# Kernel optimization log

Measured on AMD Instinct MI355X. Metric: run time of the kernel, lower is better.

## Reference

```python
import jax, jax.numpy as jnp
import numpy as np

N = 16384   # nodes at current level
M = 8192    # nodes at next (coarser) level
E = 524288  # edges (avg degree 32)
D = 128     # in_feats == out_feats
LN_EPS = 1e-5


def setup_inputs() -> dict:
    key = jax.random.key(0)
    ks = jax.random.split(key, 10)
    curr_h = jax.random.normal(ks[0], (N, D), jnp.float32)
    next_h = jax.random.normal(ks[1], (M, D), jnp.float32)
    curr_inc = jax.random.uniform(ks[2], (N, M), jnp.float32)
    edge_src = jax.random.randint(ks[3], (E,), 0, N, jnp.int32)
    edge_dst = jax.random.randint(ks[4], (E,), 0, N, jnp.int32)
    Wc = jax.random.normal(ks[5], (D, D), jnp.float32) / np.float32(np.sqrt(D))
    Wf = jax.random.normal(ks[6], (D, D), jnp.float32) / np.float32(np.sqrt(D))
    bc = jnp.zeros((D,), jnp.float32)
    bf = jnp.zeros((D,), jnp.float32)
    conv_w = jax.random.uniform(ks[7], (D,), jnp.float32)
    topDown_w = jax.random.uniform(ks[8], (D,), jnp.float32)
    gamma = jnp.ones((D,), jnp.float32)
    beta = jnp.zeros((D,), jnp.float32)
    return dict(curr_h=curr_h, next_h=next_h, curr_inc=curr_inc,
                Wc=Wc, bc=bc, Wf=Wf, bf=bf, conv_w=conv_w,
                topDown_w=topDown_w, gamma=gamma, beta=beta,
                edge_src=edge_src, edge_dst=edge_dst)


def _graph_conv(x, W, b, src, dst, n):
    # DGL GraphConv, norm='both', on graph with self-loops added.
    ones = jnp.ones(src.shape[0], x.dtype)
    out_deg = jax.ops.segment_sum(ones, src, num_segments=n) + 1.0  # +1 self-loop
    in_deg = jax.ops.segment_sum(ones, dst, num_segments=n) + 1.0
    xn = x * jax.lax.rsqrt(out_deg)[:, None]
    # neighbor SpMM + self-loop contribution
    agg = jax.ops.segment_sum(xn[src], dst, num_segments=n) + xn
    agg = agg * jax.lax.rsqrt(in_deg)[:, None]
    return agg @ W + b


def reference(curr_h, next_h, curr_inc, Wc, bc, Wf, bf, conv_w,
              topDown_w, gamma, beta, edge_src, edge_dst):
    n = curr_h.shape[0]
    conv_layer = _graph_conv(curr_h, Wc, bc, edge_src, edge_dst, n) * conv_w[None, :]
    fused_in = curr_inc @ next_h  # dense incidence matmul [N, D]
    top_down = _graph_conv(fused_in, Wf, bf, edge_src, edge_dst, n) * topDown_w[None, :]
    res = (conv_layer + top_down) * 0.5  # update == 'MEAN' over stack of 2
    # LayerNorm over feature dim
    mu = jnp.mean(res, axis=-1, keepdims=True)
    var = jnp.mean(jnp.square(res - mu), axis=-1, keepdims=True)
    res = (res - mu) * jax.lax.rsqrt(var + LN_EPS) * gamma + beta
    res = jax.nn.relu(res)  # activation == 'RELU'
    # dropout: eval mode -> identity
    return res
```

## Files before the change

kernel.cpp:

```cpp
#include <hip/hip_runtime.h>

constexpr int Nn = 16384;
constexpr int Mm = 8192;
constexpr int Ee = 524288;
constexpr int Dd = 128;

typedef __attribute__((ext_vector_type(8))) short short8v;
typedef __attribute__((ext_vector_type(4))) short short4v;
typedef __attribute__((ext_vector_type(4))) float float4v;

static __device__ __forceinline__ short f2bf(float f) {
    unsigned u = __builtin_bit_cast(unsigned, f);
    u += 0x7fffu + ((u >> 16) & 1u);
    return (short)(u >> 16);
}

__global__ void k_zero_i(int* __restrict__ p, int n) {
    int i = blockIdx.x * 256 + threadIdx.x;
    if (i < n) p[i] = 0;
}

__global__ void k_deg_count(const int* __restrict__ src, const int* __restrict__ dst,
                            int* __restrict__ cnt_out, int* __restrict__ cnt_in) {
    int e = blockIdx.x * 256 + threadIdx.x;
    if (e < Ee) {
        atomicAdd(&cnt_out[src[e]], 1);
        atomicAdd(&cnt_in[dst[e]], 1);
    }
}

__global__ void k_deg_fin(const int* __restrict__ cnt_out, const int* __restrict__ cnt_in,
                          float* __restrict__ rs_out, float* __restrict__ rs_in) {
    int i = blockIdx.x * 256 + threadIdx.x;
    if (i < Nn) {
        rs_out[i] = rsqrtf((float)(cnt_out[i] + 1));
        rs_in[i]  = rsqrtf((float)(cnt_in[i] + 1));
    }
}

__global__ void k_scan(const int* __restrict__ cnt, int* __restrict__ row_start) {
    __shared__ int s[1024];
    int t = threadIdx.x;
    int base = t * 16;
    int local[16];
    int sum = 0;
#pragma unroll
    for (int i = 0; i < 16; i++) { local[i] = cnt[base + i]; sum += local[i]; }
    s[t] = sum;
    __syncthreads();
    for (int off = 1; off < 1024; off <<= 1) {
        int v = (t >= off) ? s[t - off] : 0;
        __syncthreads();
        s[t] += v;
        __syncthreads();
    }
    int run = s[t] - sum;
#pragma unroll
    for (int i = 0; i < 16; i++) { row_start[base + i] = run; run += local[i]; }
    if (t == 1023) row_start[16384] = s[1023];
}

__global__ void k_fill(const int* __restrict__ src, const int* __restrict__ dst,
                       const int* __restrict__ row_start, int* __restrict__ cursor,
                       int* __restrict__ ebuf) {
    int e = blockIdx.x * 256 + threadIdx.x;
    if (e < Ee) {
        int d = dst[e];
        int pos = atomicAdd(&cursor[d], 1);
        ebuf[row_start[d] + pos] = src[e];
    }
}

__global__ void k_agg(const float* __restrict__ x, const float* __restrict__ rs_o,
                      const float* __restrict__ rs_i, const int* __restrict__ row_start,
                      const int* __restrict__ ebuf, float* __restrict__ agg) {
    int d = blockIdx.x * 4 + (threadIdx.x >> 6);
    int lane = threadIdx.x & 63;
    int c = lane * 2;
    int beg = row_start[d], end = row_start[d + 1];
    float ax = 0.f, ay = 0.f;
    int i = beg;
    for (; i + 1 < end; i += 2) {
        int s0 = ebuf[i], s1 = ebuf[i + 1];
        float r0 = rs_o[s0], r1 = rs_o[s1];
        float2 v0 = *(const float2*)(x + (size_t)s0 * 128 + c);
        float2 v1 = *(const float2*)(x + (size_t)s1 * 128 + c);
        ax += v0.x * r0 + v1.x * r1;
        ay += v0.y * r0 + v1.y * r1;
    }
    if (i < end) {
        int s0 = ebuf[i];
        float r0 = rs_o[s0];
        float2 v0 = *(const float2*)(x + (size_t)s0 * 128 + c);
        ax += v0.x * r0;
        ay += v0.y * r0;
    }
    float2 vs = *(const float2*)(x + (size_t)d * 128 + c);
    float ro = rs_o[d], ri = rs_i[d];
    float2 o;
    o.x = (ax + vs.x * ro) * ri;
    o.y = (ay + vs.y * ro) * ri;
    *(float2*)(agg + (size_t)d * 128 + c) = o;
}

__global__ void k_bt(const float* __restrict__ B, short* __restrict__ Bt) {
    __shared__ short T[32][40];
    int kt = blockIdx.x & 255;
    int nt = blockIdx.x >> 8;
    int t = threadIdx.x;
    int r = t >> 3;
    int c4 = (t & 7) * 4;
    float4 v = *(const float4*)(B + (size_t)(kt * 32 + r) * 128 + nt * 32 + c4);
    T[c4 + 0][r] = f2bf(v.x);
    T[c4 + 1][r] = f2bf(v.y);
    T[c4 + 2][r] = f2bf(v.z);
    T[c4 + 3][r] = f2bf(v.w);
    __syncthreads();
    int nl = t >> 3, ks = (t & 7) * 4;
    *(short4v*)(Bt + (size_t)(nt * 32 + nl) * 8192 + kt * 32 + ks) =
        *(const short4v*)(&T[nl][ks]);
}

__launch_bounds__(256, 2)
__global__ void k_mfma_gemm(const float* __restrict__ A, const short* __restrict__ Bt,
                            float* __restrict__ C) {
    __shared__ short As[32 * 72];
    __shared__ short Bs[128 * 72];

    const int tid = threadIdx.x;
    const int lane = tid & 63;
    const int wv = tid >> 6;
    const int row0 = blockIdx.x * 32;

    const int ar = tid >> 3;
    const int ak = (tid & 7) * 8;
    const float* Ap = A + (size_t)(row0 + ar) * Mm + ak;

    const int bn = tid >> 1;
    const int bk = (tid & 1) * 32;
    const short* Bp = Bt + (size_t)bn * Mm + bk;

    const int fm = lane & 15;
    const int fk = (lane >> 4) * 8;

    float4v acc[2][2] = {};

    for (int k0 = 0; k0 < Mm; k0 += 64) {
        float4 a0 = *(const float4*)(Ap + k0);
        float4 a1 = *(const float4*)(Ap + k0 + 4);
        short8v b0 = *(const short8v*)(Bp + k0);
        short8v b1 = *(const short8v*)(Bp + k0 + 8);
        short8v b2 = *(const short8v*)(Bp + k0 + 16);
        short8v b3 = *(const short8v*)(Bp + k0 + 24);
        __syncthreads();
        short8v ap;
        ap[0] = f2bf(a0.x); ap[1] = f2bf(a0.y); ap[2] = f2bf(a0.z); ap[3] = f2bf(a0.w);
        ap[4] = f2bf(a1.x); ap[5] = f2bf(a1.y); ap[6] = f2bf(a1.z); ap[7] = f2bf(a1.w);
        *(short8v*)(&As[ar * 72 + ak]) = ap;
        *(short8v*)(&Bs[bn * 72 + bk +  0]) = b0;
        *(short8v*)(&Bs[bn * 72 + bk +  8]) = b1;
        *(short8v*)(&Bs[bn * 72 + bk + 16]) = b2;
        *(short8v*)(&Bs[bn * 72 + bk + 24]) = b3;
        __syncthreads();
#pragma unroll
        for (int ks = 0; ks < 2; ks++) {
            const int kk = ks * 32 + fk;
            short8v a0f = *(const short8v*)(&As[fm * 72 + kk]);
            short8v a1f = *(const short8v*)(&As[(16 + fm) * 72 + kk]);
            short8v b0f = *(const short8v*)(&Bs[(wv * 32 + fm) * 72 + kk]);
            short8v b1f = *(const short8v*)(&Bs[(wv * 32 + 16 + fm) * 72 + kk]);
            acc[0][0] = __builtin_amdgcn_mfma_f32_16x16x32_bf16(a0f, b0f, acc[0][0], 0, 0, 0);
            acc[0][1] = __builtin_amdgcn_mfma_f32_16x16x32_bf16(a0f, b1f, acc[0][1], 0, 0, 0);
            acc[1][0] = __builtin_amdgcn_mfma_f32_16x16x32_bf16(a1f, b0f, acc[1][0], 0, 0, 0);
            acc[1][1] = __builtin_amdgcn_mfma_f32_16x16x32_bf16(a1f, b1f, acc[1][1], 0, 0, 0);
        }
    }

    const int crow = (lane >> 4) * 4;
#pragma unroll
    for (int mt = 0; mt < 2; mt++)
#pragma unroll
        for (int nt = 0; nt < 2; nt++)
#pragma unroll
            for (int r = 0; r < 4; r++)
                C[(size_t)(row0 + mt * 16 + crow + r) * 128 + wv * 32 + nt * 16 + fm] =
                    acc[mt][nt][r];
}

__launch_bounds__(256, 2)
__global__ void k_gemm(const float* __restrict__ A, const float* __restrict__ B,
                       float* __restrict__ C, int K,
                       const float* __restrict__ bias, const float* __restrict__ scale,
                       const float* __restrict__ prev, int mode) {
    __shared__ float As[32 * 36];
    __shared__ float Bs[32 * 128];

    const int tid = threadIdx.x;
    const int tx = tid & 31;
    const int ty = tid >> 5;
    const int c4 = tx * 4;
    const int r0 = ty * 4;
    const int row0 = blockIdx.x * 32;

    const int ar = tid >> 3;
    const int ak = (tid & 7) * 4;
    const float* Arow = A + (size_t)(row0 + ar) * K + ak;

    float acc[4][4] = {};

    for (int k0 = 0; k0 < K; k0 += 32) {
        float4 av = *(const float4*)(Arow + k0);
        float4 bv[4];
#pragma unroll
        for (int t = 0; t < 4; t++) {
            int idx = tid + t * 256;
            int br = idx >> 5, bc = (idx & 31) * 4;
            bv[t] = *(const float4*)(B + (size_t)(k0 + br) * 128 + bc);
        }
        __syncthreads();
        As[(ak + 0) * 36 + ar] = av.x;
        As[(ak + 1) * 36 + ar] = av.y;
        As[(ak + 2) * 36 + ar] = av.z;
        As[(ak + 3) * 36 + ar] = av.w;
#pragma unroll
        for (int t = 0; t < 4; t++) {
            int idx = tid + t * 256;
            int br = idx >> 5, bc = (idx & 31) * 4;
            *(float4*)(Bs + br * 128 + bc) = bv[t];
        }
        __syncthreads();
#pragma unroll
        for (int kk = 0; kk < 32; kk++) {
            float4 a4 = *(const float4*)(As + kk * 36 + r0);
            float4 b4 = *(const float4*)(Bs + kk * 128 + c4);
            float a[4] = {a4.x, a4.y, a4.z, a4.w};
            float b[4] = {b4.x, b4.y, b4.z, b4.w};
#pragma unroll
            for (int i = 0; i < 4; i++)
#pragma unroll
                for (int j = 0; j < 4; j++)
                    acc[i][j] = fmaf(a[i], b[j], acc[i][j]);
        }
    }

    float4 bi = *(const float4*)(bias + c4);
    float4 sc = *(const float4*)(scale + c4);
#pragma unroll
    for (int i = 0; i < 4; i++) {
        size_t o = (size_t)(row0 + r0 + i) * 128 + c4;
        float4 v = {acc[i][0], acc[i][1], acc[i][2], acc[i][3]};
        v.x = (v.x + bi.x) * sc.x;
        v.y = (v.y + bi.y) * sc.y;
        v.z = (v.z + bi.z) * sc.z;
        v.w = (v.w + bi.w) * sc.w;
        if (mode == 2) {
            float4 p = *(const float4*)(prev + o);
            v.x = (v.x + p.x) * 0.5f;
            v.y = (v.y + p.y) * 0.5f;
            v.z = (v.z + p.z) * 0.5f;
            v.w = (v.w + p.w) * 0.5f;
        }
        *(float4*)(C + o) = v;
    }
}

__global__ void k_ln_relu(const float* __restrict__ x, const float* __restrict__ gamma,
                          const float* __restrict__ beta, float* __restrict__ out) {
    int wave = threadIdx.x >> 6;
    int lane = threadIdx.x & 63;
    int row = blockIdx.x * 4 + wave;
    const float* xr = x + (size_t)row * 128;
    float2 v = *(const float2*)(xr + lane * 2);
    float s1 = v.x + v.y;
    float s2 = v.x * v.x + v.y * v.y;
#pragma unroll
    for (int m = 32; m >= 1; m >>= 1) {
        s1 += __shfl_xor(s1, m);
        s2 += __shfl_xor(s2, m);
    }
    float mu = s1 * (1.0f / 128.0f);
    float var = s2 * (1.0f / 128.0f) - mu * mu;
    float inv = rsqrtf(var + 1e-5f);
    float2 g = *(const float2*)(gamma + lane * 2);
    float2 b = *(const float2*)(beta + lane * 2);
    float2 o;
    o.x = fmaxf((v.x - mu) * inv * g.x + b.x, 0.0f);
    o.y = fmaxf((v.y - mu) * inv * g.y + b.y, 0.0f);
    *(float2*)(out + (size_t)row * 128 + lane * 2) = o;
}

extern "C" void kernel_launch(void* const* d_in, const int* in_sizes, int n_in,
                              void* d_out, int out_size, void* d_ws, size_t ws_size,
                              hipStream_t stream) {
    const float* curr_h    = (const float*)d_in[0];
    const float* next_h    = (const float*)d_in[1];
    const float* curr_inc  = (const float*)d_in[2];
    const float* Wc        = (const float*)d_in[3];
    const float* bc        = (const float*)d_in[4];
    const float* Wf        = (const float*)d_in[5];
    const float* bf        = (const float*)d_in[6];
    const float* conv_w    = (const float*)d_in[7];
    const float* topDown_w = (const float*)d_in[8];
    const float* gamma     = (const float*)d_in[9];
    const float* beta      = (const float*)d_in[10];
    const int*   esrc      = (const int*)d_in[11];
    const int*   edst      = (const int*)d_in[12];
    float* out = (float*)d_out;

    char* w = (char*)d_ws;
    int*   cnt_out = (int*)w;    w += (size_t)Nn * 4;
    int*   cnt_in  = (int*)w;    w += (size_t)Nn * 4;
    int*   cursor  = (int*)w;    w += (size_t)Nn * 4;
    int*   row_st  = (int*)w;    w += (size_t)16388 * 4;
    int*   ebuf    = (int*)w;    w += (size_t)Ee * 4;
    float* rs_out  = (float*)w;  w += (size_t)Nn * 4;
    float* rs_in   = (float*)w;  w += (size_t)Nn * 4;
    short* Bt      = (short*)w;  w += (size_t)Dd * Mm * 2;
    float* fused   = (float*)w;  w += (size_t)Nn * Dd * 4;
    float* agg     = (float*)w;  w += (size_t)Nn * Dd * 4;
    float* path    = (float*)w;  w += (size_t)Nn * Dd * 4;

    k_zero_i<<<(3 * Nn + 255) / 256, 256, 0, stream>>>(cnt_out, 3 * Nn);
    k_deg_count<<<Ee / 256, 256, 0, stream>>>(esrc, edst, cnt_out, cnt_in);
    k_deg_fin<<<Nn / 256, 256, 0, stream>>>(cnt_out, cnt_in, rs_out, rs_in);
    k_scan<<<1, 1024, 0, stream>>>(cnt_in, row_st);
    k_fill<<<Ee / 256, 256, 0, stream>>>(esrc, edst, row_st, cursor, ebuf);

    k_bt<<<1024, 256, 0, stream>>>(next_h, Bt);
    k_mfma_gemm<<<Nn / 32, 256, 0, stream>>>(curr_inc, Bt, fused);

    k_agg<<<Nn / 4, 256, 0, stream>>>(curr_h, rs_out, rs_in, row_st, ebuf, agg);
    k_gemm<<<Nn / 32, 256, 0, stream>>>(agg, Wc, path, Dd, bc, conv_w, nullptr, 1);

    k_agg<<<Nn / 4, 256, 0, stream>>>(fused, rs_out, rs_in, row_st, ebuf, agg);
    k_gemm<<<Nn / 32, 256, 0, stream>>>(agg, Wf, path, Dd, bf, topDown_w, path, 2);

    k_ln_relu<<<Nn / 4, 256, 0, stream>>>(path, gamma, beta, out);
}
```

Measured before the change: 997.0 us.

## Fuse both graph-conv paths into one aggregation and stacked GEMM with LayerNorm epilogue

Folds the conv_w/topDown_w scales into stacked weights so the two graph convolutions become a single K=256 GEMM over concatenated aggregates. A combined gather kernel processes both feature sets per edge, and the LayerNorm+ReLU runs in the GEMM epilogue. The main incidence MFMA GEMM also gets register double-buffered global loads. This removes two launches and several intermediate round trips to memory, at the cost of a wider aggregate buffer and more register pressure.

Result: faster. 960.4 us (-3.7%).

```diff
diff --git a/kernel.cpp b/kernel.cpp
--- a/kernel.cpp
+++ b/kernel.cpp
@@ -71,36 +71,59 @@
     }
 }
 
-__global__ void k_agg(const float* __restrict__ x, const float* __restrict__ rs_o,
-                      const float* __restrict__ rs_i, const int* __restrict__ row_start,
-                      const int* __restrict__ ebuf, float* __restrict__ agg) {
+__global__ void k_prep(const float* __restrict__ Wc, const float* __restrict__ Wf,
+                       const float* __restrict__ bc, const float* __restrict__ bf,
+                       const float* __restrict__ cw, const float* __restrict__ tw,
+                       float* __restrict__ Wp, float* __restrict__ bp) {
+    int i = blockIdx.x * 256 + threadIdx.x;
+    int r = i >> 7, j = i & 127;
+    float w = (r < 128) ? Wc[r * 128 + j] * cw[j] : Wf[(r - 128) * 128 + j] * tw[j];
+    Wp[i] = w;
+    if (i < 128) bp[i] = bc[i] * cw[i] + bf[i] * tw[i];
+}
+
+__global__ void k_agg2(const float* __restrict__ x1, const float* __restrict__ x2,
+                       const float* __restrict__ rs_o, const float* __restrict__ rs_i,
+                       const int* __restrict__ row_start, const int* __restrict__ ebuf,
+                       float* __restrict__ agg) {
     int d = blockIdx.x * 4 + (threadIdx.x >> 6);
     int lane = threadIdx.x & 63;
     int c = lane * 2;
     int beg = row_start[d], end = row_start[d + 1];
-    float ax = 0.f, ay = 0.f;
+    float ax = 0.f, ay = 0.f, bx = 0.f, by = 0.f;
     int i = beg;
     for (; i + 1 < end; i += 2) {
         int s0 = ebuf[i], s1 = ebuf[i + 1];
         float r0 = rs_o[s0], r1 = rs_o[s1];
-        float2 v0 = *(const float2*)(x + (size_t)s0 * 128 + c);
-        float2 v1 = *(const float2*)(x + (size_t)s1 * 128 + c);
-        ax += v0.x * r0 + v1.x * r1;
-        ay += v0.y * r0 + v1.y * r1;
+        float2 u0 = *(const float2*)(x1 + (size_t)s0 * 128 + c);
+        float2 u1 = *(const float2*)(x1 + (size_t)s1 * 128 + c);
+        float2 w0 = *(const float2*)(x2 + (size_t)s0 * 128 + c);
+        float2 w1 = *(const float2*)(x2 + (size_t)s1 * 128 + c);
+        ax += u0.x * r0 + u1.x * r1;
+        ay += u0.y * r0 + u1.y * r1;
+        bx += w0.x * r0 + w1.x * r1;
+        by += w0.y * r0 + w1.y * r1;
     }
     if (i < end) {
         int s0 = ebuf[i];
         float r0 = rs_o[s0];
-        float2 v0 = *(const float2*)(x + (size_t)s0 * 128 + c);
-        ax += v0.x * r0;
-        ay += v0.y * r0;
-    }
-    float2 vs = *(const float2*)(x + (size_t)d * 128 + c);
+        float2 u0 = *(const float2*)(x1 + (size_t)s0 * 128 + c);
+        float2 w0 = *(const float2*)(x2 + (size_t)s0 * 128 + c);
+        ax += u0.x * r0;
+        ay += u0.y * r0;
+        bx += w0.x * r0;
+        by += w0.y * r0;
+    }
+    float2 us = *(const float2*)(x1 + (size_t)d * 128 + c);
+    float2 ws = *(const float2*)(x2 + (size_t)d * 128 + c);
     float ro = rs_o[d], ri = rs_i[d];
-    float2 o;
-    o.x = (ax + vs.x * ro) * ri;
-    o.y = (ay + vs.y * ro) * ri;
-    *(float2*)(agg + (size_t)d * 128 + c) = o;
+    float2 o1, o2;
+    o1.x = (ax + us.x * ro) * ri;
+    o1.y = (ay + us.y * ro) * ri;
+    o2.x = (bx + ws.x * ro) * ri;
+    o2.y = (by + ws.y * ro) * ri;
+    *(float2*)(agg + (size_t)d * 256 + c) = o1;
+    *(float2*)(agg + (size_t)d * 256 + 128 + c) = o2;
 }
 
 __global__ void k_bt(const float* __restrict__ B, short* __restrict__ Bt) {
@@ -145,36 +168,55 @@
 
     float4v acc[2][2] = {};
 
-    for (int k0 = 0; k0 < Mm; k0 += 64) {
-        float4 a0 = *(const float4*)(Ap + k0);
-        float4 a1 = *(const float4*)(Ap + k0 + 4);
-        short8v b0 = *(const short8v*)(Bp + k0);
-        short8v b1 = *(const short8v*)(Bp + k0 + 8);
-        short8v b2 = *(const short8v*)(Bp + k0 + 16);
-        short8v b3 = *(const short8v*)(Bp + k0 + 24);
-        __syncthreads();
-        short8v ap;
-        ap[0] = f2bf(a0.x); ap[1] = f2bf(a0.y); ap[2] = f2bf(a0.z); ap[3] = f2bf(a0.w);
-        ap[4] = f2bf(a1.x); ap[5] = f2bf(a1.y); ap[6] = f2bf(a1.z); ap[7] = f2bf(a1.w);
-        *(short8v*)(&As[ar * 72 + ak]) = ap;
-        *(short8v*)(&Bs[bn * 72 + bk +  0]) = b0;
-        *(short8v*)(&Bs[bn * 72 + bk +  8]) = b1;
-        *(short8v*)(&Bs[bn * 72 + bk + 16]) = b2;
-        *(short8v*)(&Bs[bn * 72 + bk + 24]) = b3;
-        __syncthreads();
-#pragma unroll
-        for (int ks = 0; ks < 2; ks++) {
-            const int kk = ks * 32 + fk;
-            short8v a0f = *(const short8v*)(&As[fm * 72 + kk]);
-            short8v a1f = *(const short8v*)(&As[(16 + fm) * 72 + kk]);
-            short8v b0f = *(const short8v*)(&Bs[(wv * 32 + fm) * 72 + kk]);
-            short8v b1f = *(const short8v*)(&Bs[(wv * 32 + 16 + fm) * 72 + kk]);
-            acc[0][0] = __builtin_amdgcn_mfma_f32_16x16x32_bf16(a0f, b0f, acc[0][0], 0, 0, 0);
-            acc[0][1] = __builtin_amdgcn_mfma_f32_16x16x32_bf16(a0f, b1f, acc[0][1], 0, 0, 0);
-            acc[1][0] = __builtin_amdgcn_mfma_f32_16x16x32_bf16(a1f, b0f, acc[1][0], 0, 0, 0);
-            acc[1][1] = __builtin_amdgcn_mfma_f32_16x16x32_bf16(a1f, b1f, acc[1][1], 0, 0, 0);
-        }
-    }
+    float4 a0A, a1A, a0B, a1B;
+    short8v b0A, b1A, b2A, b3A, b0B, b1B, b2B, b3B;
+
+#define LOADSET(s, koff)                                   \
+    a0##s = *(const float4*)(Ap + (koff));                 \
+    a1##s = *(const float4*)(Ap + (koff) + 4);             \
+    b0##s = *(const short8v*)(Bp + (koff));                \
+    b1##s = *(const short8v*)(Bp + (koff) + 8);            \
+    b2##s = *(const short8v*)(Bp + (koff) + 16);           \
+    b3##s = *(const short8v*)(Bp + (koff) + 24);
+
+#define PHASE(s, knext)                                                        \
+    {                                                                          \
+        short8v ap;                                                            \
+        ap[0] = f2bf(a0##s.x); ap[1] = f2bf(a0##s.y);                          \
+        ap[2] = f2bf(a0##s.z); ap[3] = f2bf(a0##s.w);                          \
+        ap[4] = f2bf(a1##s.x); ap[5] = f2bf(a1##s.y);                          \
+        ap[6] = f2bf(a1##s.z); ap[7] = f2bf(a1##s.w);                          \
+        __syncthreads();                      \
+        *(short8v*)(&As[ar * 72 + ak]) = ap;                                   \
+        *(short8v*)(&Bs[bn * 72 + bk +  0]) = b0##s;                           \
+        *(short8v*)(&Bs[bn * 72 + bk +  8]) = b1##s;                           \
+        *(short8v*)(&Bs[bn * 72 + bk + 16]) = b2##s;                           \
+        *(short8v*)(&Bs[bn * 72 + bk + 24]) = b3##s;                           \
+        __syncthreads();                                                       \
+        if ((knext) < Mm) { LOADSET(s, knext) }                                \
+        _Pragma("unroll")                                                      \
+        for (int ks = 0; ks < 2; ks++) {                                       \
+            const int kk = ks * 32 + fk;                                       \
+            short8v a0f = *(const short8v*)(&As[fm * 72 + kk]);                \
+            short8v a1f = *(const short8v*)(&As[(16 + fm) * 72 + kk]);         \
+            short8v b0f = *(const short8v*)(&Bs[(wv * 32 + fm) * 72 + kk]);    \
+            short8v b1f = *(const short8v*)(&Bs[(wv * 32 + 16 + fm) * 72 + kk]); \
+            acc[0][0] = __builtin_amdgcn_mfma_f32_16x16x32_bf16(a0f, b0f, acc[0][0], 0, 0, 0); \
+            acc[0][1] = __builtin_amdgcn_mfma_f32_16x16x32_bf16(a0f, b1f, acc[0][1], 0, 0, 0); \
+            acc[1][0] = __builtin_amdgcn_mfma_f32_16x16x32_bf16(a1f, b0f, acc[1][0], 0, 0, 0); \
+            acc[1][1] = __builtin_amdgcn_mfma_f32_16x16x32_bf16(a1f, b1f, acc[1][1], 0, 0, 0); \
+        }                                                                      \
+    }
+
+    LOADSET(A, 0)
+    LOADSET(B, 64)
+
+    for (int k0 = 0; k0 < Mm; k0 += 128) {
+        PHASE(A, k0 + 128)
+        PHASE(B, k0 + 192)
+    }
+#undef PHASE
+#undef LOADSET
 
     const int crow = (lane >> 4) * 4;
 #pragma unroll
@@ -188,10 +230,10 @@
 }
 
 __launch_bounds__(256, 2)
-__global__ void k_gemm(const float* __restrict__ A, const float* __restrict__ B,
-                       float* __restrict__ C, int K,
-                       const float* __restrict__ bias, const float* __restrict__ scale,
-                       const float* __restrict__ prev, int mode) {
+__global__ void k_gemm_ln(const float* __restrict__ A, const float* __restrict__ B,
+                          const float* __restrict__ bias,
+                          const float* __restrict__ gamma, const float* __restrict__ beta,
+                          float* __restrict__ out) {
     __shared__ float As[32 * 36];
     __shared__ float Bs[32 * 128];
 
@@ -204,11 +246,11 @@
 
     const int ar = tid >> 3;
     const int ak = (tid & 7) * 4;
-    const float* Arow = A + (size_t)(row0 + ar) * K + ak;
+    const float* Arow = A + (size_t)(row0 + ar) * 256 + ak;
 
     float acc[4][4] = {};
 
-    for (int k0 = 0; k0 < K; k0 += 32) {
+    for (int k0 = 0; k0 < 256; k0 += 32) {
         float4 av = *(const float4*)(Arow + k0);
         float4 bv[4];
 #pragma unroll
@@ -244,49 +286,31 @@
     }
 
     float4 bi = *(const float4*)(bias + c4);
-    float4 sc = *(const float4*)(scale + c4);
+    float4 g  = *(const float4*)(gamma + c4);
+    float4 be = *(const float4*)(beta + c4);
 #pragma unroll
     for (int i = 0; i < 4; i++) {
-        size_t o = (size_t)(row0 + r0 + i) * 128 + c4;
-        float4 v = {acc[i][0], acc[i][1], acc[i][2], acc[i][3]};
-        v.x = (v.x + bi.x) * sc.x;
-        v.y = (v.y + bi.y) * sc.y;
-        v.z = (v.z + bi.z) * sc.z;
-        v.w = (v.w + bi.w) * sc.w;
-        if (mode == 2) {
-            float4 p = *(const float4*)(prev + o);
-            v.x = (v.x + p.x) * 0.5f;
-            v.y = (v.y + p.y) * 0.5f;
-            v.z = (v.z + p.z) * 0.5f;
-            v.w = (v.w + p.w) * 0.5f;
+        float v0 = (acc[i][0] + bi.x) * 0.5f;
+        float v1 = (acc[i][1] + bi.y) * 0.5f;
+        float v2 = (acc[i][2] + bi.z) * 0.5f;
+        float v3 = (acc[i][3] + bi.w) * 0.5f;
+        float s1 = v0 + v1 + v2 + v3;
+        float s2 = v0 * v0 + v1 * v1 + v2 * v2 + v3 * v3;
+#pragma unroll
+        for (int m = 16; m >= 1; m >>= 1) {
+            s1 += __shfl_xor(s1, m);
+            s2 += __shfl_xor(s2, m);
         }
-        *(float4*)(C + o) = v;
-    }
-}
-
-__global__ void k_ln_relu(const float* __restrict__ x, const float* __restrict__ gamma,
-                          const float* __restrict__ beta, float* __restrict__ out) {
-    int wave = threadIdx.x >> 6;
-    int lane = threadIdx.x & 63;
-    int row = blockIdx.x * 4 + wave;
-    const float* xr = x + (size_t)row * 128;
-    float2 v = *(const float2*)(xr + lane * 2);
-    float s1 = v.x + v.y;
-    float s2 = v.x * v.x + v.y * v.y;
-#pragma unroll
-    for (int m = 32; m >= 1; m >>= 1) {
-        s1 += __shfl_xor(s1, m);
-        s2 += __shfl_xor(s2, m);
-    }
-    float mu = s1 * (1.0f / 128.0f);
-    float var = s2 * (1.0f / 128.0f) - mu * mu;
-    float inv = rsqrtf(var + 1e-5f);
-    float2 g = *(const float2*)(gamma + lane * 2);
-    float2 b = *(const float2*)(beta + lane * 2);
-    float2 o;
-    o.x = fmaxf((v.x - mu) * inv * g.x + b.x, 0.0f);
-    o.y = fmaxf((v.y - mu) * inv * g.y + b.y, 0.0f);
-    *(float2*)(out + (size_t)row * 128 + lane * 2) = o;
+        float mu  = s1 * (1.0f / 128.0f);
+        float var = s2 * (1.0f / 128.0f) - mu * mu;
+        float inv = rsqrtf(var + 1e-5f);
+        float4 o;
+        o.x = fmaxf((v0 - mu) * inv * g.x + be.x, 0.0f);
+        o.y = fmaxf((v1 - mu) * inv * g.y + be.y, 0.0f);
+        o.z = fmaxf((v2 - mu) * inv * g.z + be.z, 0.0f);
+        o.w = fmaxf((v3 - mu) * inv * g.w + be.w, 0.0f);
+        *(float4*)(out + (size_t)(row0 + r0 + i) * 128 + c4) = o;
+    }
 }
 
 extern "C" void kernel_launch(void* const* d_in, const int* in_sizes, int n_in,
@@ -317,23 +341,20 @@
     float* rs_in   = (float*)w;  w += (size_t)Nn * 4;
     short* Bt      = (short*)w;  w += (size_t)Dd * Mm * 2;
     float* fused   = (float*)w;  w += (size_t)Nn * Dd * 4;
-    float* agg     = (float*)w;  w += (size_t)Nn * Dd * 4;
-    float* path    = (float*)w;  w += (size_t)Nn * Dd * 4;
+    float* agg2    = (float*)w;  w += (size_t)Nn * 256 * 4;
+    float* Wp      = (float*)w;  w += (size_t)256 * 128 * 4;
+    float* bp      = (float*)w;  w += (size_t)1024;
 
     k_zero_i<<<(3 * Nn + 255) / 256, 256, 0, stream>>>(cnt_out, 3 * Nn);
     k_deg_count<<<Ee / 256, 256, 0, stream>>>(esrc, edst, cnt_out, cnt_in);
     k_deg_fin<<<Nn / 256, 256, 0, stream>>>(cnt_out, cnt_in, rs_out, rs_in);
     k_scan<<<1, 1024, 0, stream>>>(cnt_in, row_st);
     k_fill<<<Ee / 256, 256, 0, stream>>>(esrc, edst, row_st, cursor, ebuf);
+    k_prep<<<128, 256, 0, stream>>>(Wc, Wf, bc, bf, conv_w, topDown_w, Wp, bp);
 
     k_bt<<<1024, 256, 0, stream>>>(next_h, Bt);
     k_mfma_gemm<<<Nn / 32, 256, 0, stream>>>(curr_inc, Bt, fused);
 
-    k_agg<<<Nn / 4, 256, 0, stream>>>(curr_h, rs_out, rs_in, row_st, ebuf, agg);
-    k_gemm<<<Nn / 32, 256, 0, stream>>>(agg, Wc, path, Dd, bc, conv_w, nullptr, 1);
-
-    k_agg<<<Nn / 4, 256, 0, stream>>>(fused, rs_out, rs_in, row_st, ebuf, agg);
-    k_gemm<<<Nn / 32, 256, 0, stream>>>(agg, Wf, path, Dd, bf, topDown_w, path, 2);
-
-    k_ln_relu<<<Nn / 4, 256, 0, stream>>>(path, gamma, beta, out);
-}
+    k_agg2<<<Nn / 4, 256, 0, stream>>>(curr_h, fused, rs_out, rs_in, row_st, ebuf, agg2);
+    k_gemm_ln<<<Nn / 32, 256, 0, stream>>>(agg2, Wp, bp, gamma, beta, out);
+}
```
